# Kernel tuning notes

Hardware: AMD Instinct MI355X
Metric: run time of the kernel (lower is better)

The kernel has to match this reference:

```python
import jax, jax.numpy as jnp
import numpy as np

B, S, H, M, T = 64, 512, 768, 512, 26


def setup_inputs() -> dict:
    key = jax.random.key(0)
    ks = jax.random.split(key, 10)
    hidden = jax.random.normal(ks[0], (B, S, H), dtype=jnp.float32)
    W1 = jax.random.normal(ks[1], (M, H), dtype=jnp.float32) * 0.02
    b1 = jnp.zeros((M,), jnp.float32)
    W2 = jax.random.normal(ks[2], (T, M), dtype=jnp.float32) * 0.02
    b2 = jnp.zeros((T,), jnp.float32)
    start_trans = jax.random.normal(ks[3], (T,), dtype=jnp.float32) * 0.1
    end_trans = jax.random.normal(ks[4], (T,), dtype=jnp.float32) * 0.1
    trans = jax.random.normal(ks[5], (T, T), dtype=jnp.float32) * 0.1
    labels = jax.random.randint(ks[6], (B, S), 0, T, dtype=jnp.int32)
    lengths = jax.random.randint(ks[7], (B,), 1, S + 1, dtype=jnp.int32)
    return dict(hidden=hidden, W1=W1, b1=b1, W2=W2, b2=b2,
                start_trans=start_trans, end_trans=end_trans, trans=trans,
                labels=labels, lengths=lengths)


def _crf_nll(emissions, labels, lengths, start_trans, end_trans, trans):
    # emissions: [B,S,T]; labels: [B,S]; lengths: [B]
    maskf = (jnp.arange(S)[None, :] < lengths[:, None]).astype(emissions.dtype)  # [B,S]

    # --- numerator: score of the gold path (torchcrf _compute_score) ---
    emit_gold = jnp.take_along_axis(emissions, labels[..., None], axis=-1)[..., 0]  # [B,S]
    trans_gold = trans[labels[:, :-1], labels[:, 1:]]  # [B,S-1]
    last_tags = jnp.take_along_axis(labels, (lengths - 1)[:, None], axis=1)[:, 0]  # [B]
    numerator = (start_trans[labels[:, 0]] + emit_gold[:, 0]
                 + jnp.sum((trans_gold + emit_gold[:, 1:]) * maskf[:, 1:], axis=1)
                 + end_trans[last_tags])  # [B]

    # --- denominator: log partition via forward algorithm (lax.scan) ---
    alpha0 = start_trans[None, :] + emissions[:, 0]  # [B,T]
    emis_t = jnp.swapaxes(emissions[:, 1:], 0, 1)    # [S-1,B,T]
    mask_t = jnp.swapaxes(maskf[:, 1:] > 0, 0, 1)    # [S-1,B] bool

    def step(alpha, xs):
        emit, m = xs
        # alpha[b,i] + trans[i,j] + emit[b,j] -> logsumexp over i
        nxt = jax.nn.logsumexp(alpha[:, :, None] + trans[None, :, :] + emit[:, None, :], axis=1)
        return jnp.where(m[:, None], nxt, alpha), None

    alpha, _ = jax.lax.scan(step, alpha0, (emis_t, mask_t))
    denominator = jax.nn.logsumexp(alpha + end_trans[None, :], axis=1)  # [B]

    llh = numerator - denominator
    return -jnp.mean(llh)  # loss = -crf(..., reduction='mean')


def reference(hidden, W1, b1, W2, b2, start_trans, end_trans, trans, labels, lengths):
    h = jnp.einsum('bsh,mh->bsm', hidden, W1) + b1      # fc1 (no activation in source)
    emissions = jnp.einsum('bsm,tm->bst', h, W2) + b2   # fc2 -> [B,S,T]
    return _crf_nll(emissions, labels, lengths, start_trans, end_trans, trans)
```

## Files before the change

### kernel.cpp

```cpp
#include <hip/hip_runtime.h>
#include <math.h>

#define Bn 64
#define Sn 512
#define Hn 768
#define Mn 512
#define Tn 26
#define TP 32

#define OFF_BC    0
#define OFF_BFRAG 32
#define OFF_EX    (32 + 12288)
#define EXSZ      ((size_t)Bn*Sn*TP)
#define OFF_ACC   (OFF_EX + EXSZ)
#define OFF_CNT   (OFF_ACC + 1)

typedef __attribute__((ext_vector_type(8)))  short bfrag;
typedef __attribute__((ext_vector_type(4)))  float f32x4;
typedef __attribute__((ext_vector_type(16))) float f32x16;

__device__ __forceinline__ short f2bf(float f) {
    unsigned u = __float_as_uint(f);
    unsigned r = (u + 0x7FFFu + ((u >> 16) & 1u)) >> 16;
    return (short)r;
}
__device__ __forceinline__ unsigned cvtpk(float a, float b) {
    unsigned r;
    asm("v_cvt_pk_bf16_f32 %0, %1, %2" : "=v"(r) : "v"(a), "v"(b));
    return r;
}
__device__ __forceinline__ void pswap(unsigned &a, unsigned &b) {
    asm("v_permlane32_swap_b32 %0, %1" : "+v"(a), "+v"(b));
}
__device__ __forceinline__ bfrag mkfrag(unsigned a, unsigned b, unsigned c, unsigned d) {
    union { unsigned u[4]; bfrag v; } x;
    x.u[0] = a; x.u[1] = b; x.u[2] = c; x.u[3] = d;
    return x.v;
}
__device__ __forceinline__ float rl(float x, int i) {
    return __uint_as_float(__builtin_amdgcn_readlane(__float_as_uint(x), i));
}

__global__ __launch_bounds__(256) void k_prep(const float* __restrict__ W1,
                                              const float* __restrict__ b1,
                                              const float* __restrict__ W2,
                                              const float* __restrict__ b2,
                                              float* __restrict__ ws) {
    const int bx = blockIdx.x;
    const int tid = threadIdx.x;
    if (bx == 48) {
        if (tid == 0) {
            ws[OFF_ACC] = 0.f;
            ((unsigned*)ws)[OFF_CNT] = 0u;
        }
        if (tid < TP) {
            float bcv = 0.f;
            if (tid < Tn) {
                float a0 = 0.f, a1 = 0.f, a2 = 0.f, a3 = 0.f;
                const float4* w2 = reinterpret_cast<const float4*>(W2 + (size_t)tid * Mn);
                const float4* bb = reinterpret_cast<const float4*>(b1);
                for (int m = 0; m < Mn / 4; ++m) {
                    float4 w = w2[m], v = bb[m];
                    a0 = fmaf(w.x, v.x, a0); a1 = fmaf(w.y, v.y, a1);
                    a2 = fmaf(w.z, v.z, a2); a3 = fmaf(w.w, v.w, a3);
                }
                bcv = b2[tid] + (a0 + a1) + (a2 + a3);
            }
            ws[OFF_BC + tid] = bcv;
        }
        return;
    }

    __shared__ float mrg[3][64][8];
    const int lane = tid & 63;
    const int wv   = tid >> 6;
    const int k0   = bx * 16;
    const int colA = lane & 15;
    const int mj   = ((lane >> 4) & 3) * 8;

    f32x4 acc0 = {0.f, 0.f, 0.f, 0.f}, acc1 = {0.f, 0.f, 0.f, 0.f};
    for (int mq = 0; mq < 4; ++mq) {
        const int m0 = wv * 128 + mq * 32;
        bfrag av, bv0, bv1;
#pragma unroll
        for (int j = 0; j < 8; ++j)
            av[j] = f2bf(W1[(size_t)(m0 + mj + j) * Hn + k0 + colA]);
        {
            const float* p = W2 + (size_t)(lane & 15) * Mn + m0 + mj;
            float4 x = *reinterpret_cast<const float4*>(p);
            float4 y = *reinterpret_cast<const float4*>(p + 4);
            bv0 = mkfrag(cvtpk(x.x, x.y), cvtpk(x.z, x.w), cvtpk(y.x, y.y), cvtpk(y.z, y.w));
        }
        {
            int c = 16 + (lane & 15);
            bfrag z = {};
            if (c < Tn) {
                const float* p = W2 + (size_t)c * Mn + m0 + mj;
                float4 x = *reinterpret_cast<const float4*>(p);
                float4 y = *reinterpret_cast<const float4*>(p + 4);
                z = mkfrag(cvtpk(x.x, x.y), cvtpk(x.z, x.w), cvtpk(y.x, y.y), cvtpk(y.z, y.w));
            }
            bv1 = z;
        }
        acc0 = __builtin_amdgcn_mfma_f32_16x16x32_bf16(av, bv0, acc0, 0, 0, 0);
        acc1 = __builtin_amdgcn_mfma_f32_16x16x32_bf16(av, bv1, acc1, 0, 0, 0);
    }

    if (wv > 0) {
#pragma unroll
        for (int i = 0; i < 4; ++i) {
            mrg[wv - 1][lane][i]     = acc0[i];
            mrg[wv - 1][lane][4 + i] = acc1[i];
        }
    }
    __syncthreads();
    if (wv == 0) {
        unsigned short* Bfo = (unsigned short*)(ws + OFF_BFRAG);
#pragma unroll
        for (int i = 0; i < 4; ++i) {
            float v0 = acc0[i] + mrg[0][lane][i]     + mrg[1][lane][i]     + mrg[2][lane][i];
            float v1 = acc1[i] + mrg[0][lane][4 + i] + mrg[1][lane][4 + i] + mrg[2][lane][4 + i];
            int k   = k0 + ((lane >> 4) & 3) * 4 + i;
            int ks2 = k >> 5;
            int fl  = ((k >> 3) & 3) * 16 + (lane & 15);
            Bfo[((size_t)(ks2 * 2 + 0) * 64 + fl) * 8 + (k & 7)] = (unsigned short)f2bf(v0);
            Bfo[((size_t)(ks2 * 2 + 1) * 64 + fl) * 8 + (k & 7)] = (unsigned short)f2bf(v1);
        }
    }
}

#define LOADK(KS, FA, FB, BV0, BV1)                                                        \
    {                                                                                      \
        const float* ap = abase + (KS) * 32;                                               \
        FA = *reinterpret_cast<const float4*>(ap);                                         \
        FB = *reinterpret_cast<const float4*>(ap + 4);                                     \
        BV0 = *reinterpret_cast<const bfrag*>(Bf + ((size_t)((KS) * 2 + 0) * 64 + l) * 8); \
        BV1 = *reinterpret_cast<const bfrag*>(Bf + ((size_t)((KS) * 2 + 1) * 64 + l) * 8); \
    }

__global__ __launch_bounds__(64, 2) void k_gemm(const float* __restrict__ hidden,
                                                const float* __restrict__ ws,
                                                float* __restrict__ Eexp) {
    const int l    = threadIdx.x;
    const int row0 = blockIdx.x * 16;
    const int arow = row0 + (l & 15);
    const int kg   = l >> 4;
    const float* abase = hidden + (size_t)arow * Hn + kg * 8;
    const unsigned short* Bf = (const unsigned short*)(ws + OFF_BFRAG);

    f32x4 acc0 = {0.f, 0.f, 0.f, 0.f}, acc1 = {0.f, 0.f, 0.f, 0.f};

    float4 fa0, fb0, fa1, fb1;
    bfrag bv00, bv01, bv10, bv11;
    LOADK(0, fa0, fb0, bv00, bv01);
    LOADK(1, fa1, fb1, bv10, bv11);

#pragma unroll 1
    for (int ks = 0; ks < 24; ks += 2) {
        float4 ta, tb; bfrag t0, t1;
        if (ks + 2 < 24) LOADK(ks + 2, ta, tb, t0, t1);
        bfrag av = mkfrag(cvtpk(fa0.x, fa0.y), cvtpk(fa0.z, fa0.w),
                          cvtpk(fb0.x, fb0.y), cvtpk(fb0.z, fb0.w));
        acc0 = __builtin_amdgcn_mfma_f32_16x16x32_bf16(av, bv00, acc0, 0, 0, 0);
        acc1 = __builtin_amdgcn_mfma_f32_16x16x32_bf16(av, bv01, acc1, 0, 0, 0);
        fa0 = ta; fb0 = tb; bv00 = t0; bv01 = t1;

        float4 ua, ub; bfrag u0, u1;
        if (ks + 3 < 24) LOADK(ks + 3, ua, ub, u0, u1);
        av = mkfrag(cvtpk(fa1.x, fa1.y), cvtpk(fa1.z, fa1.w),
                    cvtpk(fb1.x, fb1.y), cvtpk(fb1.z, fb1.w));
        acc0 = __builtin_amdgcn_mfma_f32_16x16x32_bf16(av, bv10, acc0, 0, 0, 0);
        acc1 = __builtin_amdgcn_mfma_f32_16x16x32_bf16(av, bv11, acc1, 0, 0, 0);
        fa1 = ua; fb1 = ub; bv10 = u0; bv11 = u1;
    }

    const int c0 = l & 15;
    const int rbase = row0 + kg * 4;
    float bc0 = ws[OFF_BC + c0], bc1 = ws[OFF_BC + 16 + c0];
#pragma unroll
    for (int i = 0; i < 4; ++i) {
        Eexp[(size_t)(rbase + i) * TP + c0]      = __expf(acc0[i] + bc0);
        Eexp[(size_t)(rbase + i) * TP + 16 + c0] = __expf(acc1[i] + bc1);
    }
}

__global__ __launch_bounds__(1024) void k_scan(const float* __restrict__ Eexp,
                                               const float* __restrict__ start_t,
                                               const float* __restrict__ end_t,
                                               const float* __restrict__ trans,
                                               const int* __restrict__ labels,
                                               const int* __restrict__ lengths,
                                               float* __restrict__ accp,
                                               unsigned* __restrict__ cntp,
                                               float* __restrict__ out) {
    __shared__ float Ech[16][32][32];
    __shared__ unsigned Qp[16][16][32];
    const int tid  = threadIdx.x;
    const int b    = blockIdx.x;
    const int len  = lengths[b];
    const int wv   = tid >> 6;
    const int lane = tid & 63;
    const int t    = lane & 31;
    const int h    = lane >> 5;

    {
        const float* Eb = Eexp + (size_t)b * Sn * TP;
        int lr = lane >> 1, hf = lane & 1;
        int s = wv * 32 + 1 + lr; s = s > 511 ? 511 : s;
        const float4* src = reinterpret_cast<const float4*>(Eb + (size_t)s * TP + hf * 16);
        float4* dst = reinterpret_cast<float4*>(&Ech[wv][lr][hf * 16]);
        dst[0] = src[0]; dst[1] = src[1]; dst[2] = src[2]; dst[3] = src[3];
    }
    __syncthreads();

    {
        const int c  = wv;
        const int s0 = c * 32;
        int nact = len - 1 - s0;
        nact = nact < 0 ? 0 : (nact > 32 ? 32 : nact);

        bfrag A0, A1, B0, B1;
#pragma unroll
        for (int j = 0; j < 8; ++j) {
            int k0 = 8 * h + j, k1 = 16 + 8 * h + j;
            A0[j] = (t < Tn && k0 < Tn) ? f2bf(__expf(trans[k0 * Tn + t]) * 0.03125f) : (short)0;
            A1[j] = (t < Tn && k1 < Tn) ? f2bf(__expf(trans[k1 * Tn + t]) * 0.03125f) : (short)0;
            B0[j] = (k0 == t) ? (short)0x3F80 : (short)0;
            B1[j] = (k1 == t) ? (short)0x3F80 : (short)0;
        }

        float qf[16];
#pragma unroll
        for (int r = 0; r < 16; ++r) {
            int row = (r & 3) + 8 * (r >> 2) + 4 * h;
            qf[r] = (row == t) ? 1.f : 0.f;
        }

        for (int j = 0; j < nact; ++j) {
            f32x16 acc = {};
            acc = __builtin_amdgcn_mfma_f32_32x32x16_bf16(A0, B0, acc, 0, 0, 0);
            acc = __builtin_amdgcn_mfma_f32_32x32x16_bf16(A1, B1, acc, 0, 0, 0);
            const float* ep = &Ech[c][j][4 * h];
            float4 e0 = *reinterpret_cast<const float4*>(ep);
            float4 e1 = *reinterpret_cast<const float4*>(ep + 8);
            float4 e2 = *reinterpret_cast<const float4*>(ep + 16);
            float4 e3 = *reinterpret_cast<const float4*>(ep + 24);
            float ev[16];
            ev[0]  = e0.x; ev[1]  = e0.y; ev[2]  = e0.z; ev[3]  = e0.w;
            ev[4]  = e1.x; ev[5]  = e1.y; ev[6]  = e1.z; ev[7]  = e1.w;
            ev[8]  = e2.x; ev[9]  = e2.y; ev[10] = e2.z; ev[11] = e2.w;
            ev[12] = e3.x; ev[13] = e3.y; ev[14] = e3.z; ev[15] = e3.w;
#pragma unroll
            for (int r = 0; r < 16; ++r) qf[r] = acc[r] * ev[r];
            if (j + 1 < nact) {
                unsigned W0 = cvtpk(qf[0],  qf[1]),  W1 = cvtpk(qf[2],  qf[3]);
                unsigned W2 = cvtpk(qf[4],  qf[5]),  W3 = cvtpk(qf[6],  qf[7]);
                unsigned W4 = cvtpk(qf[8],  qf[9]),  W5 = cvtpk(qf[10], qf[11]);
                unsigned W6 = cvtpk(qf[12], qf[13]), W7 = cvtpk(qf[14], qf[15]);
                pswap(W0, W2); pswap(W1, W3); pswap(W4, W6); pswap(W5, W7);
                B0 = mkfrag(W0, W1, W2, W3);
                B1 = mkfrag(W4, W5, W6, W7);
            }
        }

#pragma unroll
        for (int g = 0; g < 4; ++g) {
            unsigned u0 = cvtpk(qf[4*g + 0], qf[4*g + 1]);
            unsigned u1 = cvtpk(qf[4*g + 2], qf[4*g + 3]);
            Qp[c][4*g + 2*h][t]     = u0;
            Qp[c][4*g + 2*h + 1][t] = u1;
        }
    }
    __syncthreads();

    if (wv == 0) {
        float alpha = (t < Tn) ? __expf(start_t[t]) * Eexp[(size_t)b * Sn * TP + t] : 0.f;
        float logZ = 0.f;
        for (int c = 0; c < 16; ++c) {
            float p0 = 0.f, p1 = 0.f, p2 = 0.f, p3 = 0.f;
#pragma unroll
            for (int p = 0; p < 16; p += 2) {
                unsigned ua = Qp[c][p][t];
                unsigned ub = Qp[c][p + 1][t];
                p0 = fmaf(rl(alpha, 2*p    ), __uint_as_float(ua << 16),          p0);
                p1 = fmaf(rl(alpha, 2*p + 1), __uint_as_float(ua & 0xFFFF0000u), p1);
                p2 = fmaf(rl(alpha, 2*p + 2), __uint_as_float(ub << 16),          p2);
                p3 = fmaf(rl(alpha, 2*p + 3), __uint_as_float(ub & 0xFFFF0000u), p3);
            }
            float v = (p0 + p1) + (p2 + p3);
            float C = __uint_as_float(__builtin_amdgcn_readfirstlane(__float_as_uint(v)));
            alpha = v / C;
            logZ += __logf(C);
        }
        float dv = (t < Tn && lane < 32) ? alpha * __expf(end_t[t]) : 0.f;
#pragma unroll
        for (int off = 32; off; off >>= 1) dv += __shfl_xor(dv, off);
        if (lane == 0) {
            float denom = logZ + __logf(dv) + (float)(len - 1) * 3.46573590279973f;
            atomicAdd(accp, -denom);
            __threadfence();
            unsigned old = atomicAdd(cntp, 1u);
            if (old == 2u * Bn - 1u) {
                float tot = atomicAdd(accp, 0.0f);
                out[0] = -tot * (1.0f / 64.0f);
            }
        }
    } else if (wv == 1) {
        const int base = b * Sn;
        float part = 0.f;
        for (int s2 = 1 + lane; s2 < len; s2 += 64) {
            int lp = labels[base + s2 - 1];
            int lc = labels[base + s2];
            int si = s2 - 1;
            part += trans[lp * Tn + lc] + __logf(Ech[si >> 5][si & 31][lc]);
        }
#pragma unroll
        for (int off = 32; off; off >>= 1) part += __shfl_xor(part, off);
        if (lane == 0) {
            int l0 = labels[base], ll = labels[base + len - 1];
            float numer = part + start_t[l0] + __logf(Eexp[(size_t)base * TP + l0]) + end_t[ll];
            atomicAdd(accp, numer);
            __threadfence();
            unsigned old = atomicAdd(cntp, 1u);
            if (old == 2u * Bn - 1u) {
                float tot = atomicAdd(accp, 0.0f);
                out[0] = -tot * (1.0f / 64.0f);
            }
        }
    }
}

extern "C" void kernel_launch(void* const* d_in, const int* in_sizes, int n_in,
                              void* d_out, int out_size, void* d_ws, size_t ws_size,
                              hipStream_t stream) {
    const float* hidden  = (const float*)d_in[0];
    const float* W1      = (const float*)d_in[1];
    const float* b1      = (const float*)d_in[2];
    const float* W2      = (const float*)d_in[3];
    const float* b2      = (const float*)d_in[4];
    const float* start_t = (const float*)d_in[5];
    const float* end_t   = (const float*)d_in[6];
    const float* trans   = (const float*)d_in[7];
    const int*   labels  = (const int*)d_in[8];
    const int*   lengths = (const int*)d_in[9];
    float* ws  = (float*)d_ws;
    float* out = (float*)d_out;

    hipLaunchKernelGGL(k_prep, dim3(49), dim3(256), 0, stream, W1, b1, W2, b2, ws);
    hipLaunchKernelGGL(k_gemm, dim3(2048), dim3(64), 0, stream, hidden, ws, ws + OFF_EX);
    hipLaunchKernelGGL(k_scan, dim3(64), dim3(1024), 0, stream, ws + OFF_EX, start_t, end_t,
                       trans, labels, lengths, ws + OFF_ACC,
                       (unsigned*)(ws + OFF_CNT), out);
}
```

Baseline: 53.62 us.

## Stage B fragments in LDS and deepen A prefetch in GEMM kernel

The GEMM kernel now uses 256-thread blocks (4 waves, 64 rows each). Each block first copies the shared bf16 B fragments (48KB) into LDS, and the waves then read B from LDS instead of global/L2. The A-operand prefetch goes from 2 to 4 k-steps in flight, with wraparound dummy loads at the end. The aim is less global traffic for B and better hiding of hidden-state load latency. The cost is a 48KB LDS copy per block plus a barrier, which may limit occupancy, and a few redundant wrap-around loads.

```diff
diff --git a/kernel.cpp b/kernel.cpp
--- a/kernel.cpp
+++ b/kernel.cpp
@@ -129,49 +129,79 @@
     }
 }
 
-#define LOADK(KS, FA, FB, BV0, BV1)                                                        \
-    {                                                                                      \
-        const float* ap = abase + (KS) * 32;                                               \
-        FA = *reinterpret_cast<const float4*>(ap);                                         \
-        FB = *reinterpret_cast<const float4*>(ap + 4);                                     \
-        BV0 = *reinterpret_cast<const bfrag*>(Bf + ((size_t)((KS) * 2 + 0) * 64 + l) * 8); \
-        BV1 = *reinterpret_cast<const bfrag*>(Bf + ((size_t)((KS) * 2 + 1) * 64 + l) * 8); \
-    }
-
-__global__ __launch_bounds__(64, 2) void k_gemm(const float* __restrict__ hidden,
-                                                const float* __restrict__ ws,
-                                                float* __restrict__ Eexp) {
-    const int l    = threadIdx.x;
-    const int row0 = blockIdx.x * 16;
+#define LA(KS, FA, FB)                                      \
+    {                                                       \
+        const float* ap = abase + (KS) * 32;                \
+        FA = *reinterpret_cast<const float4*>(ap);          \
+        FB = *reinterpret_cast<const float4*>(ap + 4);      \
+    }
+
+__global__ __launch_bounds__(256, 2) void k_gemm(const float* __restrict__ hidden,
+                                                 const float* __restrict__ ws,
+                                                 float* __restrict__ Eexp) {
+    __shared__ short Bl[24576];
+    const int tid = threadIdx.x;
+    const int l   = tid & 63;
+    const int wv  = tid >> 6;
+
+    {
+        const float4* src = reinterpret_cast<const float4*>(ws + OFF_BFRAG);
+        float4* dst = reinterpret_cast<float4*>(Bl);
+        for (int i = tid; i < 3072; i += 256) dst[i] = src[i];
+    }
+    __syncthreads();
+
+    const int row0 = blockIdx.x * 64 + wv * 16;
     const int arow = row0 + (l & 15);
     const int kg   = l >> 4;
     const float* abase = hidden + (size_t)arow * Hn + kg * 8;
-    const unsigned short* Bf = (const unsigned short*)(ws + OFF_BFRAG);
+    const short* Bf = Bl;
 
     f32x4 acc0 = {0.f, 0.f, 0.f, 0.f}, acc1 = {0.f, 0.f, 0.f, 0.f};
 
-    float4 fa0, fb0, fa1, fb1;
-    bfrag bv00, bv01, bv10, bv11;
-    LOADK(0, fa0, fb0, bv00, bv01);
-    LOADK(1, fa1, fb1, bv10, bv11);
+    float4 fa0, fb0, fa1, fb1, fa2, fb2, fa3, fb3;
+    LA(0, fa0, fb0); LA(1, fa1, fb1); LA(2, fa2, fb2); LA(3, fa3, fb3);
 
 #pragma unroll 1
-    for (int ks = 0; ks < 24; ks += 2) {
-        float4 ta, tb; bfrag t0, t1;
-        if (ks + 2 < 24) LOADK(ks + 2, ta, tb, t0, t1);
-        bfrag av = mkfrag(cvtpk(fa0.x, fa0.y), cvtpk(fa0.z, fa0.w),
-                          cvtpk(fb0.x, fb0.y), cvtpk(fb0.z, fb0.w));
-        acc0 = __builtin_amdgcn_mfma_f32_16x16x32_bf16(av, bv00, acc0, 0, 0, 0);
-        acc1 = __builtin_amdgcn_mfma_f32_16x16x32_bf16(av, bv01, acc1, 0, 0, 0);
-        fa0 = ta; fb0 = tb; bv00 = t0; bv01 = t1;
-
-        float4 ua, ub; bfrag u0, u1;
-        if (ks + 3 < 24) LOADK(ks + 3, ua, ub, u0, u1);
+    for (int ks = 0; ks < 24; ks += 4) {
+        int kp;
+        bfrag bv0, bv1, av;
+
+        bv0 = *reinterpret_cast<const bfrag*>(Bf + ((ks * 2 + 0) * 64 + l) * 8);
+        bv1 = *reinterpret_cast<const bfrag*>(Bf + ((ks * 2 + 1) * 64 + l) * 8);
+        av = mkfrag(cvtpk(fa0.x, fa0.y), cvtpk(fa0.z, fa0.w),
+                    cvtpk(fb0.x, fb0.y), cvtpk(fb0.z, fb0.w));
+        kp = ks + 4; kp = kp < 24 ? kp : 0;
+        LA(kp, fa0, fb0);
+        acc0 = __builtin_amdgcn_mfma_f32_16x16x32_bf16(av, bv0, acc0, 0, 0, 0);
+        acc1 = __builtin_amdgcn_mfma_f32_16x16x32_bf16(av, bv1, acc1, 0, 0, 0);
+
+        bv0 = *reinterpret_cast<const bfrag*>(Bf + (((ks + 1) * 2 + 0) * 64 + l) * 8);
+        bv1 = *reinterpret_cast<const bfrag*>(Bf + (((ks + 1) * 2 + 1) * 64 + l) * 8);
         av = mkfrag(cvtpk(fa1.x, fa1.y), cvtpk(fa1.z, fa1.w),
                     cvtpk(fb1.x, fb1.y), cvtpk(fb1.z, fb1.w));
-        acc0 = __builtin_amdgcn_mfma_f32_16x16x32_bf16(av, bv10, acc0, 0, 0, 0);
-        acc1 = __builtin_amdgcn_mfma_f32_16x16x32_bf16(av, bv11, acc1, 0, 0, 0);
-        fa1 = ua; fb1 = ub; bv10 = u0; bv11 = u1;
+        kp = ks + 5; kp = kp < 24 ? kp : 0;
+        LA(kp, fa1, fb1);
+        acc0 = __builtin_amdgcn_mfma_f32_16x16x32_bf16(av, bv0, acc0, 0, 0, 0);
+        acc1 = __builtin_amdgcn_mfma_f32_16x16x32_bf16(av, bv1, acc1, 0, 0, 0);
+
+        bv0 = *reinterpret_cast<const bfrag*>(Bf + (((ks + 2) * 2 + 0) * 64 + l) * 8);
+        bv1 = *reinterpret_cast<const bfrag*>(Bf + (((ks + 2) * 2 + 1) * 64 + l) * 8);
+        av = mkfrag(cvtpk(fa2.x, fa2.y), cvtpk(fa2.z, fa2.w),
+                    cvtpk(fb2.x, fb2.y), cvtpk(fb2.z, fb2.w));
+        kp = ks + 6; kp = kp < 24 ? kp : 0;
+        LA(kp, fa2, fb2);
+        acc0 = __builtin_amdgcn_mfma_f32_16x16x32_bf16(av, bv0, acc0, 0, 0, 0);
+        acc1 = __builtin_amdgcn_mfma_f32_16x16x32_bf16(av, bv1, acc1, 0, 0, 0);
+
+        bv0 = *reinterpret_cast<const bfrag*>(Bf + (((ks + 3) * 2 + 0) * 64 + l) * 8);
+        bv1 = *reinterpret_cast<const bfrag*>(Bf + (((ks + 3) * 2 + 1) * 64 + l) * 8);
+        av = mkfrag(cvtpk(fa3.x, fa3.y), cvtpk(fa3.z, fa3.w),
+                    cvtpk(fb3.x, fb3.y), cvtpk(fb3.z, fb3.w));
+        kp = ks + 7; kp = kp < 24 ? kp : 0;
+        LA(kp, fa3, fb3);
+        acc0 = __builtin_amdgcn_mfma_f32_16x16x32_bf16(av, bv0, acc0, 0, 0, 0);
+        acc1 = __builtin_amdgcn_mfma_f32_16x16x32_bf16(av, bv1, acc1, 0, 0, 0);
     }
 
     const int c0 = l & 15;
@@ -347,7 +377,7 @@
     float* out = (float*)d_out;
 
     hipLaunchKernelGGL(k_prep, dim3(49), dim3(256), 0, stream, W1, b1, W2, b2, ws);
-    hipLaunchKernelGGL(k_gemm, dim3(2048), dim3(64), 0, stream, hidden, ws, ws + OFF_EX);
+    hipLaunchKernelGGL(k_gemm, dim3(512), dim3(256), 0, stream, hidden, ws, ws + OFF_EX);
     hipLaunchKernelGGL(k_scan, dim3(64), dim3(1024), 0, stream, ws + OFF_EX, start_t, end_t,
                        trans, labels, lengths, ws + OFF_ACC,
                        (unsigned*)(ws + OFF_CNT), out);
```

New measurement: 76.91 us. 1.43x slower.

## Stage hidden rows through swizzled LDS for coalesced GEMM loads

Applied to the files above, without the earlier changes.

The GEMM kernel now loads 16 full hidden rows per wave in 256-float chunks, with each lane reading a contiguous float4 so global reads are coalesced. The chunks are written into an XOR-swizzled shared-memory tile and then read back in MFMA fragment order. Blocks grow to 4 waves covering 64 rows each, and the grid shrinks accordingly. The intent is to replace the strided per-lane 32-byte reads with row-contiguous loads. In exchange it adds LDS traffic, more register pressure from 16 float4 loads in flight, and less overlap between loads and compute within a chunk.

```diff
diff --git a/kernel.cpp b/kernel.cpp
--- a/kernel.cpp
+++ b/kernel.cpp
@@ -129,49 +129,52 @@
     }
 }
 
-#define LOADK(KS, FA, FB, BV0, BV1)                                                        \
-    {                                                                                      \
-        const float* ap = abase + (KS) * 32;                                               \
-        FA = *reinterpret_cast<const float4*>(ap);                                         \
-        FB = *reinterpret_cast<const float4*>(ap + 4);                                     \
-        BV0 = *reinterpret_cast<const bfrag*>(Bf + ((size_t)((KS) * 2 + 0) * 64 + l) * 8); \
-        BV1 = *reinterpret_cast<const bfrag*>(Bf + ((size_t)((KS) * 2 + 1) * 64 + l) * 8); \
-    }
-
-__global__ __launch_bounds__(64, 2) void k_gemm(const float* __restrict__ hidden,
-                                                const float* __restrict__ ws,
-                                                float* __restrict__ Eexp) {
-    const int l    = threadIdx.x;
-    const int row0 = blockIdx.x * 16;
-    const int arow = row0 + (l & 15);
+__global__ __launch_bounds__(256, 2) void k_gemm(const float* __restrict__ hidden,
+                                                 const float* __restrict__ ws,
+                                                 float* __restrict__ Eexp) {
+    __shared__ float4 At[4][16][64];
+    const int tid  = threadIdx.x;
+    const int l    = tid & 63;
+    const int wv   = tid >> 6;
+    const int row0 = blockIdx.x * 64 + wv * 16;
+    const int r    = l & 15;
     const int kg   = l >> 4;
-    const float* abase = hidden + (size_t)arow * Hn + kg * 8;
     const unsigned short* Bf = (const unsigned short*)(ws + OFF_BFRAG);
 
     f32x4 acc0 = {0.f, 0.f, 0.f, 0.f}, acc1 = {0.f, 0.f, 0.f, 0.f};
 
-    float4 fa0, fb0, fa1, fb1;
-    bfrag bv00, bv01, bv10, bv11;
-    LOADK(0, fa0, fb0, bv00, bv01);
-    LOADK(1, fa1, fb1, bv10, bv11);
+    bfrag bv0 = *reinterpret_cast<const bfrag*>(Bf + ((size_t)0 * 64 + l) * 8);
+    bfrag bv1 = *reinterpret_cast<const bfrag*>(Bf + ((size_t)1 * 64 + l) * 8);
+
+    const int xr = ((r << 1) | (r >> 2)) & 7;
+    const float* grow = hidden + (size_t)row0 * Hn;
 
 #pragma unroll 1
-    for (int ks = 0; ks < 24; ks += 2) {
-        float4 ta, tb; bfrag t0, t1;
-        if (ks + 2 < 24) LOADK(ks + 2, ta, tb, t0, t1);
-        bfrag av = mkfrag(cvtpk(fa0.x, fa0.y), cvtpk(fa0.z, fa0.w),
-                          cvtpk(fb0.x, fb0.y), cvtpk(fb0.z, fb0.w));
-        acc0 = __builtin_amdgcn_mfma_f32_16x16x32_bf16(av, bv00, acc0, 0, 0, 0);
-        acc1 = __builtin_amdgcn_mfma_f32_16x16x32_bf16(av, bv01, acc1, 0, 0, 0);
-        fa0 = ta; fb0 = tb; bv00 = t0; bv01 = t1;
-
-        float4 ua, ub; bfrag u0, u1;
-        if (ks + 3 < 24) LOADK(ks + 3, ua, ub, u0, u1);
-        av = mkfrag(cvtpk(fa1.x, fa1.y), cvtpk(fa1.z, fa1.w),
-                    cvtpk(fb1.x, fb1.y), cvtpk(fb1.z, fb1.w));
-        acc0 = __builtin_amdgcn_mfma_f32_16x16x32_bf16(av, bv10, acc0, 0, 0, 0);
-        acc1 = __builtin_amdgcn_mfma_f32_16x16x32_bf16(av, bv11, acc1, 0, 0, 0);
-        fa1 = ua; fb1 = ub; bv10 = u0; bv11 = u1;
+    for (int ch = 0; ch < 3; ++ch) {
+        float4 va[16];
+#pragma unroll
+        for (int i = 0; i < 16; ++i)
+            va[i] = *reinterpret_cast<const float4*>(grow + (size_t)i * Hn + ch * 256 + l * 4);
+#pragma unroll
+        for (int i = 0; i < 16; ++i) {
+            const int xi = ((i << 1) | (i >> 2)) & 7;
+            At[wv][i][l ^ xi] = va[i];
+        }
+#pragma unroll
+        for (int ksL = 0; ksL < 8; ++ksL) {
+            const int ksg = ch * 8 + ksL;
+            const int nk = (ksg + 1 < 24) ? ksg + 1 : 0;
+            bfrag nb0 = *reinterpret_cast<const bfrag*>(Bf + ((size_t)(nk * 2 + 0) * 64 + l) * 8);
+            bfrag nb1 = *reinterpret_cast<const bfrag*>(Bf + ((size_t)(nk * 2 + 1) * 64 + l) * 8);
+            const int c = ksL * 8 + kg * 2;
+            float4 fa = At[wv][r][c ^ xr];
+            float4 fb = At[wv][r][(c + 1) ^ xr];
+            bfrag av = mkfrag(cvtpk(fa.x, fa.y), cvtpk(fa.z, fa.w),
+                              cvtpk(fb.x, fb.y), cvtpk(fb.z, fb.w));
+            acc0 = __builtin_amdgcn_mfma_f32_16x16x32_bf16(av, bv0, acc0, 0, 0, 0);
+            acc1 = __builtin_amdgcn_mfma_f32_16x16x32_bf16(av, bv1, acc1, 0, 0, 0);
+            bv0 = nb0; bv1 = nb1;
+        }
     }
 
     const int c0 = l & 15;
@@ -347,7 +350,7 @@
     float* out = (float*)d_out;
 
     hipLaunchKernelGGL(k_prep, dim3(49), dim3(256), 0, stream, W1, b1, W2, b2, ws);
-    hipLaunchKernelGGL(k_gemm, dim3(2048), dim3(64), 0, stream, hidden, ws, ws + OFF_EX);
+    hipLaunchKernelGGL(k_gemm, dim3(512), dim3(256), 0, stream, hidden, ws, ws + OFF_EX);
     hipLaunchKernelGGL(k_scan, dim3(64), dim3(1024), 0, stream, ws + OFF_EX, start_t, end_t,
                        trans, labels, lengths, ws + OFF_ACC,
                        (unsigned*)(ws + OFF_CNT), out);
```

Measured after the change: 55.04 us. 1.03x slower.

## Fuse emission GEMM into CRF scan kernel, keeping emissions in LDS

Applied to the files above, without the earlier changes.

Removes the separate GEMM kernel. Each batch block of 1024 threads now computes its own 512x32 exponentiated emission tile with MFMA and writes it straight into shared memory. The forward scan and the gold-path score then read from there. This avoids one kernel launch and the global write and read of the emission buffer. In exchange, the whole hidden-state stream (about 100 MB) is read by only 64 workgroups instead of 2048, which may leave much of the GPU idle and limit memory bandwidth.

```diff
diff --git a/kernel.cpp b/kernel.cpp
--- a/kernel.cpp
+++ b/kernel.cpp
@@ -10,9 +10,7 @@
 
 #define OFF_BC    0
 #define OFF_BFRAG 32
-#define OFF_EX    (32 + 12288)
-#define EXSZ      ((size_t)Bn*Sn*TP)
-#define OFF_ACC   (OFF_EX + EXSZ)
+#define OFF_ACC   (32 + 12288)
 #define OFF_CNT   (OFF_ACC + 1)
 
 typedef __attribute__((ext_vector_type(8)))  short bfrag;
@@ -138,84 +136,84 @@
         BV1 = *reinterpret_cast<const bfrag*>(Bf + ((size_t)((KS) * 2 + 1) * 64 + l) * 8); \
     }
 
-__global__ __launch_bounds__(64, 2) void k_gemm(const float* __restrict__ hidden,
-                                                const float* __restrict__ ws,
-                                                float* __restrict__ Eexp) {
-    const int l    = threadIdx.x;
-    const int row0 = blockIdx.x * 16;
-    const int arow = row0 + (l & 15);
-    const int kg   = l >> 4;
-    const float* abase = hidden + (size_t)arow * Hn + kg * 8;
-    const unsigned short* Bf = (const unsigned short*)(ws + OFF_BFRAG);
-
-    f32x4 acc0 = {0.f, 0.f, 0.f, 0.f}, acc1 = {0.f, 0.f, 0.f, 0.f};
-
-    float4 fa0, fb0, fa1, fb1;
-    bfrag bv00, bv01, bv10, bv11;
-    LOADK(0, fa0, fb0, bv00, bv01);
-    LOADK(1, fa1, fb1, bv10, bv11);
-
-#pragma unroll 1
-    for (int ks = 0; ks < 24; ks += 2) {
-        float4 ta, tb; bfrag t0, t1;
-        if (ks + 2 < 24) LOADK(ks + 2, ta, tb, t0, t1);
-        bfrag av = mkfrag(cvtpk(fa0.x, fa0.y), cvtpk(fa0.z, fa0.w),
-                          cvtpk(fb0.x, fb0.y), cvtpk(fb0.z, fb0.w));
-        acc0 = __builtin_amdgcn_mfma_f32_16x16x32_bf16(av, bv00, acc0, 0, 0, 0);
-        acc1 = __builtin_amdgcn_mfma_f32_16x16x32_bf16(av, bv01, acc1, 0, 0, 0);
-        fa0 = ta; fb0 = tb; bv00 = t0; bv01 = t1;
-
-        float4 ua, ub; bfrag u0, u1;
-        if (ks + 3 < 24) LOADK(ks + 3, ua, ub, u0, u1);
-        av = mkfrag(cvtpk(fa1.x, fa1.y), cvtpk(fa1.z, fa1.w),
-                    cvtpk(fb1.x, fb1.y), cvtpk(fb1.z, fb1.w));
-        acc0 = __builtin_amdgcn_mfma_f32_16x16x32_bf16(av, bv10, acc0, 0, 0, 0);
-        acc1 = __builtin_amdgcn_mfma_f32_16x16x32_bf16(av, bv11, acc1, 0, 0, 0);
-        fa1 = ua; fb1 = ub; bv10 = u0; bv11 = u1;
-    }
-
-    const int c0 = l & 15;
-    const int rbase = row0 + kg * 4;
-    float bc0 = ws[OFF_BC + c0], bc1 = ws[OFF_BC + 16 + c0];
-#pragma unroll
-    for (int i = 0; i < 4; ++i) {
-        Eexp[(size_t)(rbase + i) * TP + c0]      = __expf(acc0[i] + bc0);
-        Eexp[(size_t)(rbase + i) * TP + 16 + c0] = __expf(acc1[i] + bc1);
-    }
-}
-
-__global__ __launch_bounds__(1024) void k_scan(const float* __restrict__ Eexp,
-                                               const float* __restrict__ start_t,
-                                               const float* __restrict__ end_t,
-                                               const float* __restrict__ trans,
-                                               const int* __restrict__ labels,
-                                               const int* __restrict__ lengths,
-                                               float* __restrict__ accp,
-                                               unsigned* __restrict__ cntp,
-                                               float* __restrict__ out) {
-    __shared__ float Ech[16][32][32];
+__global__ __launch_bounds__(1024, 1) void k_main(const float* __restrict__ hidden,
+                                                  const float* __restrict__ ws,
+                                                  const float* __restrict__ start_t,
+                                                  const float* __restrict__ end_t,
+                                                  const float* __restrict__ trans,
+                                                  const int* __restrict__ labels,
+                                                  const int* __restrict__ lengths,
+                                                  float* __restrict__ accp,
+                                                  unsigned* __restrict__ cntp,
+                                                  float* __restrict__ out) {
+    __shared__ float El[Sn][32];
     __shared__ unsigned Qp[16][16][32];
+
     const int tid  = threadIdx.x;
     const int b    = blockIdx.x;
     const int len  = lengths[b];
     const int wv   = tid >> 6;
     const int lane = tid & 63;
-    const int t    = lane & 31;
-    const int h    = lane >> 5;
+    const int l    = lane;
+    const int kg   = l >> 4;
+    const int c0   = l & 15;
+    const unsigned short* Bf = (const unsigned short*)(ws + OFF_BFRAG);
 
     {
-        const float* Eb = Eexp + (size_t)b * Sn * TP;
-        int lr = lane >> 1, hf = lane & 1;
-        int s = wv * 32 + 1 + lr; s = s > 511 ? 511 : s;
-        const float4* src = reinterpret_cast<const float4*>(Eb + (size_t)s * TP + hf * 16);
-        float4* dst = reinterpret_cast<float4*>(&Ech[wv][lr][hf * 16]);
-        dst[0] = src[0]; dst[1] = src[1]; dst[2] = src[2]; dst[3] = src[3];
+        const float bc0 = ws[OFF_BC + c0], bc1 = ws[OFF_BC + 16 + c0];
+#pragma unroll 1
+        for (int tile = 0; tile < 2; ++tile) {
+            const int lrow0 = wv * 32 + tile * 16;
+            const float* abase = hidden + ((size_t)b * Sn + lrow0 + (l & 15)) * Hn + kg * 8;
+
+            f32x4 acc0 = {0.f, 0.f, 0.f, 0.f}, acc1 = {0.f, 0.f, 0.f, 0.f};
+            float4 fa0, fb0, fa1, fb1;
+            bfrag bv00, bv01, bv10, bv11;
+            LOADK(0, fa0, fb0, bv00, bv01);
+            LOADK(1, fa1, fb1, bv10, bv11);
+
+#pragma unroll 1
+            for (int ks = 0; ks < 22; ks += 2) {
+                float4 ta, tb; bfrag t0, t1;
+                LOADK(ks + 2, ta, tb, t0, t1);
+                bfrag av = mkfrag(cvtpk(fa0.x, fa0.y), cvtpk(fa0.z, fa0.w),
+                                  cvtpk(fb0.x, fb0.y), cvtpk(fb0.z, fb0.w));
+                acc0 = __builtin_amdgcn_mfma_f32_16x16x32_bf16(av, bv00, acc0, 0, 0, 0);
+                acc1 = __builtin_amdgcn_mfma_f32_16x16x32_bf16(av, bv01, acc1, 0, 0, 0);
+                fa0 = ta; fb0 = tb; bv00 = t0; bv01 = t1;
+
+                float4 ua, ub; bfrag u0, u1;
+                LOADK(ks + 3, ua, ub, u0, u1);
+                av = mkfrag(cvtpk(fa1.x, fa1.y), cvtpk(fa1.z, fa1.w),
+                            cvtpk(fb1.x, fb1.y), cvtpk(fb1.z, fb1.w));
+                acc0 = __builtin_amdgcn_mfma_f32_16x16x32_bf16(av, bv10, acc0, 0, 0, 0);
+                acc1 = __builtin_amdgcn_mfma_f32_16x16x32_bf16(av, bv11, acc1, 0, 0, 0);
+                fa1 = ua; fb1 = ub; bv10 = u0; bv11 = u1;
+            }
+            {
+                bfrag av = mkfrag(cvtpk(fa0.x, fa0.y), cvtpk(fa0.z, fa0.w),
+                                  cvtpk(fb0.x, fb0.y), cvtpk(fb0.z, fb0.w));
+                acc0 = __builtin_amdgcn_mfma_f32_16x16x32_bf16(av, bv00, acc0, 0, 0, 0);
+                acc1 = __builtin_amdgcn_mfma_f32_16x16x32_bf16(av, bv01, acc1, 0, 0, 0);
+                av = mkfrag(cvtpk(fa1.x, fa1.y), cvtpk(fa1.z, fa1.w),
+                            cvtpk(fb1.x, fb1.y), cvtpk(fb1.z, fb1.w));
+                acc0 = __builtin_amdgcn_mfma_f32_16x16x32_bf16(av, bv10, acc0, 0, 0, 0);
+                acc1 = __builtin_amdgcn_mfma_f32_16x16x32_bf16(av, bv11, acc1, 0, 0, 0);
+            }
+            const int rb = lrow0 + kg * 4;
+#pragma unroll
+            for (int i = 0; i < 4; ++i) {
+                El[rb + i][c0]      = __expf(acc0[i] + bc0);
+                El[rb + i][16 + c0] = __expf(acc1[i] + bc1);
+            }
+        }
     }
     __syncthreads();
 
     {
-        const int c  = wv;
-        const int s0 = c * 32;
+        const int t = lane & 31;
+        const int h = lane >> 5;
+        const int s0 = wv * 32;
         int nact = len - 1 - s0;
         nact = nact < 0 ? 0 : (nact > 32 ? 32 : nact);
 
@@ -240,7 +238,7 @@
             f32x16 acc = {};
             acc = __builtin_amdgcn_mfma_f32_32x32x16_bf16(A0, B0, acc, 0, 0, 0);
             acc = __builtin_amdgcn_mfma_f32_32x32x16_bf16(A1, B1, acc, 0, 0, 0);
-            const float* ep = &Ech[c][j][4 * h];
+            const float* ep = &El[s0 + 1 + j][4 * h];
             float4 e0 = *reinterpret_cast<const float4*>(ep);
             float4 e1 = *reinterpret_cast<const float4*>(ep + 8);
             float4 e2 = *reinterpret_cast<const float4*>(ep + 16);
@@ -267,14 +265,15 @@
         for (int g = 0; g < 4; ++g) {
             unsigned u0 = cvtpk(qf[4*g + 0], qf[4*g + 1]);
             unsigned u1 = cvtpk(qf[4*g + 2], qf[4*g + 3]);
-            Qp[c][4*g + 2*h][t]     = u0;
-            Qp[c][4*g + 2*h + 1][t] = u1;
+            Qp[wv][4*g + 2*(lane >> 5)][lane & 31]     = u0;
+            Qp[wv][4*g + 2*(lane >> 5) + 1][lane & 31] = u1;
         }
     }
     __syncthreads();
 
     if (wv == 0) {
-        float alpha = (t < Tn) ? __expf(start_t[t]) * Eexp[(size_t)b * Sn * TP + t] : 0.f;
+        const int t = lane & 31;
+        float alpha = (t < Tn) ? __expf(start_t[t]) * El[0][t] : 0.f;
         float logZ = 0.f;
         for (int c = 0; c < 16; ++c) {
             float p0 = 0.f, p1 = 0.f, p2 = 0.f, p3 = 0.f;
@@ -311,14 +310,13 @@
         for (int s2 = 1 + lane; s2 < len; s2 += 64) {
             int lp = labels[base + s2 - 1];
             int lc = labels[base + s2];
-            int si = s2 - 1;
-            part += trans[lp * Tn + lc] + __logf(Ech[si >> 5][si & 31][lc]);
+            part += trans[lp * Tn + lc] + __logf(El[s2][lc]);
         }
 #pragma unroll
         for (int off = 32; off; off >>= 1) part += __shfl_xor(part, off);
         if (lane == 0) {
             int l0 = labels[base], ll = labels[base + len - 1];
-            float numer = part + start_t[l0] + __logf(Eexp[(size_t)base * TP + l0]) + end_t[ll];
+            float numer = part + start_t[l0] + __logf(El[0][l0]) + end_t[ll];
             atomicAdd(accp, numer);
             __threadfence();
             unsigned old = atomicAdd(cntp, 1u);
@@ -347,8 +345,7 @@
     float* out = (float*)d_out;
 
     hipLaunchKernelGGL(k_prep, dim3(49), dim3(256), 0, stream, W1, b1, W2, b2, ws);
-    hipLaunchKernelGGL(k_gemm, dim3(2048), dim3(64), 0, stream, hidden, ws, ws + OFF_EX);
-    hipLaunchKernelGGL(k_scan, dim3(64), dim3(1024), 0, stream, ws + OFF_EX, start_t, end_t,
+    hipLaunchKernelGGL(k_main, dim3(64), dim3(1024), 0, stream, hidden, ws, start_t, end_t,
                        trans, labels, lengths, ws + OFF_ACC,
                        (unsigned*)(ws + OFF_CNT), out);
 }
```

New measurement: 88.43 us. 64.9% more time.
